# Optimization experiments

Measured on AMD Instinct MI355X. Metric: run time of the kernel, lower is better.

Reference implementation:

```python
import jax, jax.numpy as jnp
import numpy as np

D = 128          # node feature dim (input_dim)
ATT_NUM = 2      # number of attention heads (att_num)
ATT_TIMES = 2    # attention refinement iterations (att_times)
K = 1            # interact_dim from att_style 'ntn_1'
DIN2 = D * ATT_NUM   # NTN input dim = 256
FMAP = 16        # feature_map_dim
B = 8            # number of graph pairs
N = 100000       # nodes per graph
EPS = 1e-12      # F.normalize eps


def _glorot(key, shape):
    fan_in, fan_out = shape[-1], shape[-2] if len(shape) > 1 else shape[-1]
    std = np.sqrt(2.0 / (fan_in + fan_out)).astype(np.float32)
    return jax.random.normal(key, shape, dtype=jnp.float32) * std


def setup_inputs() -> dict:
    key = jax.random.key(0)
    ks = jax.random.split(key, 16)
    inp = {
        "x1": jax.random.normal(ks[0], (B, N, D), dtype=jnp.float32),
        "x2": jax.random.normal(ks[1], (B, N, D), dtype=jnp.float32),
        # Attention params (stacked over att_num heads)
        "W_att": _glorot(ks[2], (ATT_NUM, D, D)),
        "V_att": _glorot(ks[3], (ATT_NUM, K, 2 * D)),
        "Wt_att": _glorot(ks[4], (ATT_NUM, K, D, D)),
        "U_att": _glorot(ks[5], (ATT_NUM, K, 1)),
        "b_att": jax.random.normal(ks[6], (ATT_NUM, K), dtype=jnp.float32) * 0.1,
        # NTN params
        "V_ntn": _glorot(ks[7], (FMAP, 2 * DIN2)),
        "W_ntn": _glorot(ks[8], (FMAP, DIN2, DIN2)),
        "b_ntn": jax.random.normal(ks[9], (FMAP,), dtype=jnp.float32),
        # projection MLP: 16 -> 8 -> 4 -> 2 -> 1 (Linear, no bias; weight shape (out, in))
        "proj0": _glorot(ks[10], (8, 16)),
        "proj1": _glorot(ks[11], (4, 8)),
        "proj2": _glorot(ks[12], (2, 4)),
        "proj3": _glorot(ks[13], (1, 2)),
    }
    return inp


def _l1_normalize(s, axis):
    return s / jnp.maximum(jnp.sum(jnp.abs(s), axis=axis, keepdims=True), EPS)


def _attention(x, W_att, V_att, Wt_att, U_att, b_att):
    # x: (N, D)  ->  pooled graph embedding (D * ATT_NUM,)
    outs = []
    for i in range(ATT_NUM):
        xc = x
        out = None
        Va, Vb = V_att[i, :, :D], V_att[i, :, D:]   # (K, D) each
        for _ in range(ATT_TIMES):
            h = jnp.tanh(jnp.mean(xc, axis=0) @ W_att[i])        # (D,)
            # NTN-style attention scores, vectorized over all nodes
            s = xc @ Va.T + (Vb @ h)[None, :]                    # (N, K)
            s = s + jnp.einsum('nd,kde,e->nk', xc, Wt_att[i], h)
            s = s + b_att[i][None, :]
            s = _l1_normalize(s, axis=1)
            att = jax.nn.sigmoid(s) @ U_att[i]                   # (N, 1)
            out = att[:, 0] @ xc                                 # (D,)
            xc = xc * att
        outs.append(out)
    return jnp.concatenate(outs)   # (DIN2,)


def _ntn(g1, g2, V_ntn, W_ntn, b_ntn):
    # g1, g2: (DIN2,) -> (FMAP,)
    Va, Vb = V_ntn[:, :DIN2], V_ntn[:, DIN2:]
    s = Va @ g1 + Vb @ g2 + jnp.einsum('fde,d,e->f', W_ntn, g1, g2) + b_ntn
    s = s / jnp.maximum(jnp.sum(jnp.abs(s)), EPS)   # L1 normalize over the single row
    return jax.nn.relu(s)


def reference(x1, x2, W_att, V_att, Wt_att, U_att, b_att,
              V_ntn, W_ntn, b_ntn, proj0, proj1, proj2, proj3):
    def pair_fn(xa, xb):
        g1 = _attention(xa, W_att, V_att, Wt_att, U_att, b_att)
        g2 = _attention(xb, W_att, V_att, Wt_att, U_att, b_att)
        y = _ntn(g1, g2, V_ntn, W_ntn, b_ntn)      # (FMAP,)
        for Wp in (proj0, proj1, proj2, proj3):
            y = Wp @ y
        return y                                    # (1,)
    return jax.vmap(pair_fn)(x1, x2)                # (B, 1) pairwise similarity scores
```

## Files before the change

### kernel.cpp

```cpp
#include <hip/hip_runtime.h>
#include <hip/hip_bf16.h>
#include <math.h>

#define NROWS 100000
#define DIM 128
#define NGRAPH 16
#define NCHUNK 128
#define CHROWS 782
#define EPSV 1e-12f

#define SZ_SUMP (NGRAPH*NCHUNK*DIM)
#define SZ_WV   (NGRAPH*2*DIM)
#define SZ_OP   (NGRAPH*NCHUNK*2*DIM)
#define OFF_SUMP 0
#define OFF_WV1 (OFF_SUMP + SZ_SUMP)
#define OFF_C1  (OFF_WV1 + SZ_WV)
#define OFF_O1P (OFF_C1 + 32)
#define OFF_WV2 (OFF_O1P + SZ_OP)
#define OFF_C2  (OFF_WV2 + SZ_WV)
#define OFF_O2P (OFF_C2 + 32)
#define OFF_S   (OFF_O2P + SZ_OP)

typedef float v4f __attribute__((ext_vector_type(4)));

__device__ __forceinline__ const float* graph_ptr(const float* x1, const float* x2, int g) {
    return (g < 8) ? (x1 + (size_t)g * NROWS * DIM) : (x2 + (size_t)(g - 8) * NROWS * DIM);
}

__device__ __forceinline__ float4 ldnt4(const float* p) {
    v4f v = __builtin_nontemporal_load(reinterpret_cast<const v4f*>(p));
    return make_float4(v.x, v.y, v.z, v.w);
}

__device__ __forceinline__ float4 ld4(const float* p) {
    return *reinterpret_cast<const float4*>(p);
}

__device__ __forceinline__ float red16(float x) {
    int t;
    t = __builtin_amdgcn_update_dpp(0, __float_as_int(x), 0xB1, 0xF, 0xF, true);
    x += __int_as_float(t);
    t = __builtin_amdgcn_update_dpp(0, __float_as_int(x), 0x4E, 0xF, 0xF, true);
    x += __int_as_float(t);
    t = __builtin_amdgcn_update_dpp(0, __float_as_int(x), 0x141, 0xF, 0xF, true);
    x += __int_as_float(t);
    t = __builtin_amdgcn_update_dpp(0, __float_as_int(x), 0x140, 0xF, 0xF, true);
    x += __int_as_float(t);
    return x;
}

__device__ __forceinline__ float dot8(float4 v0, float4 v1, float4 w0, float4 w1) {
    float d = v0.x * w0.x;
    d = fmaf(v0.y, w0.y, d); d = fmaf(v0.z, w0.z, d); d = fmaf(v0.w, w0.w, d);
    d = fmaf(v1.x, w1.x, d); d = fmaf(v1.y, w1.y, d); d = fmaf(v1.z, w1.z, d);
    d = fmaf(v1.w, w1.w, d);
    return d;
}

__device__ __forceinline__ void acc4(float4& a, float f, float4 v) {
    a.x = fmaf(f, v.x, a.x); a.y = fmaf(f, v.y, a.y);
    a.z = fmaf(f, v.z, a.z); a.w = fmaf(f, v.w, a.w);
}

__global__ __launch_bounds__(256, 8) void k_sum(const float* __restrict__ x1,
                                                const float* __restrict__ x2,
                                                float* __restrict__ sump) {
    int g = blockIdx.x >> 7, c = blockIdx.x & (NCHUNK - 1);
    const float* xg = graph_ptr(x1, x2, g);
    int lane = threadIdx.x & 31, grp = threadIdx.x >> 5;
    int col = lane * 4;
    float ax = 0.f, ay = 0.f, az = 0.f, aw = 0.f;
    int r0 = c * CHROWS, r1 = min(r0 + CHROWS, NROWS);
    int r = r0 + grp;
    for (; r + 24 < r1; r += 32) {
        float4 a = ldnt4(xg + (size_t)r * DIM + col);
        float4 b = ldnt4(xg + (size_t)(r + 8) * DIM + col);
        float4 d = ldnt4(xg + (size_t)(r + 16) * DIM + col);
        float4 e = ldnt4(xg + (size_t)(r + 24) * DIM + col);
        ax += a.x; ay += a.y; az += a.z; aw += a.w;
        ax += b.x; ay += b.y; az += b.z; aw += b.w;
        ax += d.x; ay += d.y; az += d.z; aw += d.w;
        ax += e.x; ay += e.y; az += e.z; aw += e.w;
    }
    for (; r < r1; r += 8) {
        float4 a = ldnt4(xg + (size_t)r * DIM + col);
        ax += a.x; ay += a.y; az += a.z; aw += a.w;
    }
    __shared__ float4 lds[256];
    lds[threadIdx.x] = make_float4(ax, ay, az, aw);
    __syncthreads();
    if (threadIdx.x < 32) {
        float4 t = lds[threadIdx.x];
        for (int k = 1; k < 8; ++k) {
            float4 o = lds[k * 32 + threadIdx.x];
            t.x += o.x; t.y += o.y; t.z += o.z; t.w += o.w;
        }
        *reinterpret_cast<float4*>(sump + ((size_t)g * NCHUNK + c) * DIM + threadIdx.x * 4) = t;
    }
}

__global__ __launch_bounds__(256) void k_prep(const float* __restrict__ src, int phase,
                                              const float* __restrict__ W_att,
                                              const float* __restrict__ V_att,
                                              const float* __restrict__ Wt_att,
                                              const float* __restrict__ b_att,
                                              float* __restrict__ wv, float* __restrict__ cc) {
    int g = blockIdx.x >> 1, i = blockIdx.x & 1;
    int tid = threadIdx.x, t = tid & 127, half = tid >> 7;
    __shared__ float mean[DIM], h[DIM], red2[256];
    __shared__ float wt[DIM][DIM + 1];
    const float* Wt = Wt_att + (size_t)i * DIM * DIM;
    for (int idx = tid; idx < DIM * DIM; idx += 256)
        wt[idx >> 7][idx & 127] = Wt[idx];
    float s = 0.f;
    if (phase == 1) {
        for (int c = half; c < NCHUNK; c += 2) s += src[((size_t)g * NCHUNK + c) * DIM + t];
    } else {
        for (int c = half; c < NCHUNK; c += 2) s += src[(((size_t)g * NCHUNK + c) * 2 + i) * DIM + t];
    }
    red2[tid] = s; __syncthreads();
    if (half == 0) mean[t] = (red2[t] + red2[t + 128]) * (1.f / (float)NROWS);
    __syncthreads();
    const float* W = W_att + (size_t)i * DIM * DIM;
    float hv = 0.f;
    for (int d = half * 64; d < half * 64 + 64; ++d) hv = fmaf(mean[d], W[d * DIM + t], hv);
    red2[tid] = hv; __syncthreads();
    if (half == 0) h[t] = tanhf(red2[t] + red2[t + 128]);
    __syncthreads();
    float w = 0.f;
    for (int e = half * 64; e < half * 64 + 64; ++e) w = fmaf(wt[t][e], h[e], w);
    red2[tid] = w; __syncthreads();
    const float* Va = V_att + (size_t)i * 2 * DIM;
    if (half == 0) wv[((size_t)g * 2 + i) * DIM + t] = Va[t] + red2[t] + red2[t + 128];
    __syncthreads();
    if (half == 0) red2[t] = Va[DIM + t] * h[t];
    __syncthreads();
    for (int k = 64; k; k >>= 1) {
        if (tid < k) red2[tid] += red2[tid + k];
        __syncthreads();
    }
    if (tid == 0) cc[g * 2 + i] = red2[0] + b_att[i];
}

__device__ __forceinline__ void body2(float4 v0, float4 v1,
                                      float4 w0a, float4 w0b, float4 w1a, float4 w1b,
                                      float cc0, float cc1,
                                      float ap0, float an0, float ap1, float an1,
                                      float4& a0l, float4& a0h, float4& a1l, float4& a1h) {
    float d0 = red16(dot8(v0, v1, w0a, w0b));
    float d1 = red16(dot8(v0, v1, w1a, w1b));
    float at0 = (d0 + cc0 >= 0.f) ? ap0 : an0;
    float at1 = (d1 + cc1 >= 0.f) ? ap1 : an1;
    acc4(a0l, at0, v0); acc4(a0h, at0, v1);
    acc4(a1l, at1, v0); acc4(a1h, at1, v1);
}

__global__ __launch_bounds__(256, 6) void k_pass2(const float* __restrict__ x1,
                                                  const float* __restrict__ x2,
                                                  const float* __restrict__ wv1,
                                                  const float* __restrict__ c1,
                                                  const float* __restrict__ U_att,
                                                  float* __restrict__ o1p) {
    int g = blockIdx.x >> 7, c = blockIdx.x & (NCHUNK - 1);
    const float* xg = graph_ptr(x1, x2, g);
    int tid = threadIdx.x;
    int l16 = tid & 15, slot = tid >> 4;
    int cb = l16 * 4;
    float4 w0a = ld4(wv1 + ((size_t)g * 2 + 0) * DIM + cb);
    float4 w0b = ld4(wv1 + ((size_t)g * 2 + 0) * DIM + 64 + cb);
    float4 w1a = ld4(wv1 + ((size_t)g * 2 + 1) * DIM + cb);
    float4 w1b = ld4(wv1 + ((size_t)g * 2 + 1) * DIM + 64 + cb);
    float cc0 = c1[g * 2 + 0], cc1 = c1[g * 2 + 1];
    float u0 = U_att[0], u1 = U_att[1];
    float sp = 1.f / (1.f + expf(-1.f)), sn = 1.f / (1.f + expf(1.f));
    float ap0 = u0 * sp, an0 = u0 * sn, ap1 = u1 * sp, an1 = u1 * sn;
    float4 a0l = make_float4(0, 0, 0, 0), a0h = make_float4(0, 0, 0, 0);
    float4 a1l = make_float4(0, 0, 0, 0), a1h = make_float4(0, 0, 0, 0);
    int r0 = c * CHROWS, r1 = min(r0 + CHROWS, NROWS);
    int r = r0 + slot;
    for (; r + 16 < r1; r += 32) {
        const float* p = xg + (size_t)r * DIM + cb;
        const float* q = xg + (size_t)(r + 16) * DIM + cb;
        float4 v0 = ldnt4(p), v1 = ldnt4(p + 64);
        float4 y0 = ldnt4(q), y1 = ldnt4(q + 64);
        body2(v0, v1, w0a, w0b, w1a, w1b, cc0, cc1, ap0, an0, ap1, an1, a0l, a0h, a1l, a1h);
        body2(y0, y1, w0a, w0b, w1a, w1b, cc0, cc1, ap0, an0, ap1, an1, a0l, a0h, a1l, a1h);
    }
    for (; r < r1; r += 16) {
        const float* p = xg + (size_t)r * DIM + cb;
        float4 v0 = ldnt4(p), v1 = ldnt4(p + 64);
        body2(v0, v1, w0a, w0b, w1a, w1b, cc0, cc1, ap0, an0, ap1, an1, a0l, a0h, a1l, a1h);
    }
    __shared__ float red[2][16][DIM];
    *reinterpret_cast<float4*>(&red[0][slot][cb]) = a0l;
    *reinterpret_cast<float4*>(&red[0][slot][64 + cb]) = a0h;
    *reinterpret_cast<float4*>(&red[1][slot][cb]) = a1l;
    *reinterpret_cast<float4*>(&red[1][slot][64 + cb]) = a1h;
    __syncthreads();
    int i = tid >> 7, d = tid & 127;
    float s = 0.f;
    #pragma unroll
    for (int k = 0; k < 16; ++k) s += red[i][k][d];
    o1p[(((size_t)g * NCHUNK + c) * 2 + i) * DIM + d] = s;
}

__device__ __forceinline__ void body3(float4 v0, float4 v1,
                                      float4 wA0a, float4 wA0b, float4 wA1a, float4 wA1b,
                                      float4 wB0a, float4 wB0b, float4 wB1a, float4 wB1b,
                                      float cA0, float cA1, float cB0, float cB1,
                                      float ap0, float an0, float ap1, float an1,
                                      float4& a0l, float4& a0h, float4& a1l, float4& a1h) {
    float dA0 = red16(dot8(v0, v1, wA0a, wA0b));
    float dA1 = red16(dot8(v0, v1, wA1a, wA1b));
    float dB0 = red16(dot8(v0, v1, wB0a, wB0b));
    float dB1 = red16(dot8(v0, v1, wB1a, wB1b));
    float at10 = (dA0 + cA0 >= 0.f) ? ap0 : an0;
    float at11 = (dA1 + cA1 >= 0.f) ? ap1 : an1;
    float at20 = (fmaf(at10, dB0, cB0) >= 0.f) ? ap0 : an0;
    float at21 = (fmaf(at11, dB1, cB1) >= 0.f) ? ap1 : an1;
    float f0 = at10 * at20, f1 = at11 * at21;
    acc4(a0l, f0, v0); acc4(a0h, f0, v1);
    acc4(a1l, f1, v0); acc4(a1h, f1, v1);
}

__global__ __launch_bounds__(256, 6) void k_pass3(const float* __restrict__ x1,
                                                  const float* __restrict__ x2,
                                                  const float* __restrict__ wv1,
                                                  const float* __restrict__ c1,
                                                  const float* __restrict__ wv2,
                                                  const float* __restrict__ c2,
                                                  const float* __restrict__ U_att,
                                                  float* __restrict__ o2p) {
    int g = blockIdx.x >> 7, c = blockIdx.x & (NCHUNK - 1);
    const float* xg = graph_ptr(x1, x2, g);
    int tid = threadIdx.x;
    int l16 = tid & 15, slot = tid >> 4;
    int cb = l16 * 4;
    float4 wA0a = ld4(wv1 + ((size_t)g * 2 + 0) * DIM + cb);
    float4 wA0b = ld4(wv1 + ((size_t)g * 2 + 0) * DIM + 64 + cb);
    float4 wA1a = ld4(wv1 + ((size_t)g * 2 + 1) * DIM + cb);
    float4 wA1b = ld4(wv1 + ((size_t)g * 2 + 1) * DIM + 64 + cb);
    float4 wB0a = ld4(wv2 + ((size_t)g * 2 + 0) * DIM + cb);
    float4 wB0b = ld4(wv2 + ((size_t)g * 2 + 0) * DIM + 64 + cb);
    float4 wB1a = ld4(wv2 + ((size_t)g * 2 + 1) * DIM + cb);
    float4 wB1b = ld4(wv2 + ((size_t)g * 2 + 1) * DIM + 64 + cb);
    float cA0 = c1[g * 2 + 0], cA1 = c1[g * 2 + 1];
    float cB0 = c2[g * 2 + 0], cB1 = c2[g * 2 + 1];
    float u0 = U_att[0], u1 = U_att[1];
    float sp = 1.f / (1.f + expf(-1.f)), sn = 1.f / (1.f + expf(1.f));
    float ap0 = u0 * sp, an0 = u0 * sn, ap1 = u1 * sp, an1 = u1 * sn;
    float4 a0l = make_float4(0, 0, 0, 0), a0h = make_float4(0, 0, 0, 0);
    float4 a1l = make_float4(0, 0, 0, 0), a1h = make_float4(0, 0, 0, 0);
    int r0 = c * CHROWS, r1 = min(r0 + CHROWS, NROWS);
    int r = r0 + slot;
    for (; r + 16 < r1; r += 32) {
        const float* p = xg + (size_t)r * DIM + cb;
        const float* q = xg + (size_t)(r + 16) * DIM + cb;
        float4 v0 = ldnt4(p), v1 = ldnt4(p + 64);
        float4 y0 = ldnt4(q), y1 = ldnt4(q + 64);
        body3(v0, v1, wA0a, wA0b, wA1a, wA1b, wB0a, wB0b, wB1a, wB1b,
              cA0, cA1, cB0, cB1, ap0, an0, ap1, an1, a0l, a0h, a1l, a1h);
        body3(y0, y1, wA0a, wA0b, wA1a, wA1b, wB0a, wB0b, wB1a, wB1b,
              cA0, cA1, cB0, cB1, ap0, an0, ap1, an1, a0l, a0h, a1l, a1h);
    }
    for (; r < r1; r += 16) {
        const float* p = xg + (size_t)r * DIM + cb;
        float4 v0 = ldnt4(p), v1 = ldnt4(p + 64);
        body3(v0, v1, wA0a, wA0b, wA1a, wA1b, wB0a, wB0b, wB1a, wB1b,
              cA0, cA1, cB0, cB1, ap0, an0, ap1, an1, a0l, a0h, a1l, a1h);
    }
    __shared__ float red[2][16][DIM];
    *reinterpret_cast<float4*>(&red[0][slot][cb]) = a0l;
    *reinterpret_cast<float4*>(&red[0][slot][64 + cb]) = a0h;
    *reinterpret_cast<float4*>(&red[1][slot][cb]) = a1l;
    *reinterpret_cast<float4*>(&red[1][slot][64 + cb]) = a1h;
    __syncthreads();
    int i = tid >> 7, d = tid & 127;
    float s = 0.f;
    #pragma unroll
    for (int k = 0; k < 16; ++k) s += red[i][k][d];
    o2p[(((size_t)g * NCHUNK + c) * 2 + i) * DIM + d] = s;
}

__global__ __launch_bounds__(256) void k_ntn(const float* __restrict__ o2p,
                                             const float* __restrict__ V_ntn,
                                             const float* __restrict__ W_ntn,
                                             const float* __restrict__ b_ntn,
                                             float* __restrict__ sout) {
    int b = blockIdx.x >> 4, f = blockIdx.x & 15;
    int e = threadIdx.x;
    __shared__ float g1s[256], g2s[256], red[256];
    int i = e >> 7, d = e & 127;
    float s1 = 0.f, s2 = 0.f;
    for (int c = 0; c < NCHUNK; ++c) {
        s1 += o2p[(((size_t)b * NCHUNK + c) * 2 + i) * DIM + d];
        s2 += o2p[(((size_t)(8 + b) * NCHUNK + c) * 2 + i) * DIM + d];
    }
    g1s[e] = s1; g2s[e] = s2;
    __syncthreads();
    const float* Wf = W_ntn + (size_t)f * 256 * 256;
    float acc = 0.f;
    for (int dd = 0; dd < 256; ++dd) acc = fmaf(Wf[(size_t)dd * 256 + e], g1s[dd], acc);
    float p = acc * g2s[e];
    p = fmaf(V_ntn[(size_t)f * 512 + e], g1s[e], p);
    p = fmaf(V_ntn[(size_t)f * 512 + 256 + e], g2s[e], p);
    red[e] = p;
    __syncthreads();
    for (int k = 128; k; k >>= 1) {
        if (e < k) red[e] += red[e + k];
        __syncthreads();
    }
    if (e == 0) sout[b * 16 + f] = red[0] + b_ntn[f];
}

__global__ __launch_bounds__(64) void k_out(const float* __restrict__ sout,
                                            const float* __restrict__ p0,
                                            const float* __restrict__ p1,
                                            const float* __restrict__ p2,
                                            const float* __restrict__ p3,
                                            float* __restrict__ out) {
    int b = blockIdx.x;
    if (threadIdx.x != 0) return;
    float s[16]; float l1 = 0.f;
    for (int f = 0; f < 16; ++f) { s[f] = sout[b * 16 + f]; l1 += fabsf(s[f]); }
    float inv = 1.f / fmaxf(l1, EPSV);
    float y[16];
    for (int f = 0; f < 16; ++f) { float t = s[f] * inv; y[f] = t > 0.f ? t : 0.f; }
    float v2[4], v1[8], P[16];
    for (int j = 0; j < 4; ++j) v2[j] = p3[0] * p2[j] + p3[1] * p2[4 + j];
    for (int j = 0; j < 8; ++j) { float a = 0.f; for (int k = 0; k < 4; ++k) a = fmaf(v2[k], p1[k * 8 + j], a); v1[j] = a; }
    for (int j = 0; j < 16; ++j) { float a = 0.f; for (int k = 0; k < 8; ++k) a = fmaf(v1[k], p0[k * 16 + j], a); P[j] = a; }
    float o = 0.f;
    for (int f = 0; f < 16; ++f) o = fmaf(P[f], y[f], o);
    out[b] = o;
}

extern "C" void kernel_launch(void* const* d_in, const int* in_sizes, int n_in,
                              void* d_out, int out_size, void* d_ws, size_t ws_size,
                              hipStream_t stream) {
    const float* x1    = (const float*)d_in[0];
    const float* x2    = (const float*)d_in[1];
    const float* W_att = (const float*)d_in[2];
    const float* V_att = (const float*)d_in[3];
    const float* Wt_att= (const float*)d_in[4];
    const float* U_att = (const float*)d_in[5];
    const float* b_att = (const float*)d_in[6];
    const float* V_ntn = (const float*)d_in[7];
    const float* W_ntn = (const float*)d_in[8];
    const float* b_ntn = (const float*)d_in[9];
    const float* p0    = (const float*)d_in[10];
    const float* p1    = (const float*)d_in[11];
    const float* p2    = (const float*)d_in[12];
    const float* p3    = (const float*)d_in[13];
    float* ws  = (float*)d_ws;
    float* out = (float*)d_out;

    k_sum<<<NGRAPH * NCHUNK, 256, 0, stream>>>(x1, x2, ws + OFF_SUMP);
    k_prep<<<NGRAPH * 2, 256, 0, stream>>>(ws + OFF_SUMP, 1, W_att, V_att, Wt_att, b_att,
                                           ws + OFF_WV1, ws + OFF_C1);
    k_pass2<<<NGRAPH * NCHUNK, 256, 0, stream>>>(x1, x2, ws + OFF_WV1, ws + OFF_C1, U_att,
                                                 ws + OFF_O1P);
    k_prep<<<NGRAPH * 2, 256, 0, stream>>>(ws + OFF_O1P, 2, W_att, V_att, Wt_att, b_att,
                                           ws + OFF_WV2, ws + OFF_C2);
    k_pass3<<<NGRAPH * NCHUNK, 256, 0, stream>>>(x1, x2, ws + OFF_WV1, ws + OFF_C1,
                                                 ws + OFF_WV2, ws + OFF_C2, U_att,
                                                 ws + OFF_O2P);
    k_ntn<<<8 * 16, 256, 0, stream>>>(ws + OFF_O2P, V_ntn, W_ntn, b_ntn, ws + OFF_S);
    k_out<<<8, 64, 0, stream>>>(ws + OFF_S, p0, p1, p2, p3, out);
}
```

Before: 486.4 us.

## Process graphs in batches of four so repeated passes hit the Infinity Cache

Splits the 16 graphs into four batches and runs the sum, prep, and two attention passes per batch, so each batch (about 200 MB) can stay resident in the last-level cache across its three reads. Nontemporal loads become regular loads so the data is retained in cache. Chunk count per graph doubles and occupancy hints are removed to keep the smaller grids filled. This adds many more kernel launches, and per-launch parallelism is lower.

```diff
diff --git a/kernel.cpp b/kernel.cpp
--- a/kernel.cpp
+++ b/kernel.cpp
@@ -5,13 +5,14 @@
 #define NROWS 100000
 #define DIM 128
 #define NGRAPH 16
-#define NCHUNK 128
-#define CHROWS 782
+#define BATCH 4
+#define CH2 256
+#define CHR2 391
 #define EPSV 1e-12f
 
-#define SZ_SUMP (NGRAPH*NCHUNK*DIM)
+#define SZ_SUMP (NGRAPH*CH2*DIM)
 #define SZ_WV   (NGRAPH*2*DIM)
-#define SZ_OP   (NGRAPH*NCHUNK*2*DIM)
+#define SZ_OP   (NGRAPH*CH2*2*DIM)
 #define OFF_SUMP 0
 #define OFF_WV1 (OFF_SUMP + SZ_SUMP)
 #define OFF_C1  (OFF_WV1 + SZ_WV)
@@ -21,15 +22,8 @@
 #define OFF_O2P (OFF_C2 + 32)
 #define OFF_S   (OFF_O2P + SZ_OP)
 
-typedef float v4f __attribute__((ext_vector_type(4)));
-
 __device__ __forceinline__ const float* graph_ptr(const float* x1, const float* x2, int g) {
     return (g < 8) ? (x1 + (size_t)g * NROWS * DIM) : (x2 + (size_t)(g - 8) * NROWS * DIM);
-}
-
-__device__ __forceinline__ float4 ldnt4(const float* p) {
-    v4f v = __builtin_nontemporal_load(reinterpret_cast<const v4f*>(p));
-    return make_float4(v.x, v.y, v.z, v.w);
 }
 
 __device__ __forceinline__ float4 ld4(const float* p) {
@@ -62,28 +56,25 @@
     a.z = fmaf(f, v.z, a.z); a.w = fmaf(f, v.w, a.w);
 }
 
-__global__ __launch_bounds__(256, 8) void k_sum(const float* __restrict__ x1,
-                                                const float* __restrict__ x2,
-                                                float* __restrict__ sump) {
-    int g = blockIdx.x >> 7, c = blockIdx.x & (NCHUNK - 1);
+__global__ __launch_bounds__(256) void k_sum(const float* __restrict__ x1,
+                                             const float* __restrict__ x2,
+                                             int gbase,
+                                             float* __restrict__ sump) {
+    int g = gbase + (blockIdx.x >> 8), c = blockIdx.x & (CH2 - 1);
     const float* xg = graph_ptr(x1, x2, g);
     int lane = threadIdx.x & 31, grp = threadIdx.x >> 5;
     int col = lane * 4;
     float ax = 0.f, ay = 0.f, az = 0.f, aw = 0.f;
-    int r0 = c * CHROWS, r1 = min(r0 + CHROWS, NROWS);
+    int r0 = c * CHR2, r1 = min(r0 + CHR2, NROWS);
     int r = r0 + grp;
-    for (; r + 24 < r1; r += 32) {
-        float4 a = ldnt4(xg + (size_t)r * DIM + col);
-        float4 b = ldnt4(xg + (size_t)(r + 8) * DIM + col);
-        float4 d = ldnt4(xg + (size_t)(r + 16) * DIM + col);
-        float4 e = ldnt4(xg + (size_t)(r + 24) * DIM + col);
+    for (; r + 8 < r1; r += 16) {
+        float4 a = ld4(xg + (size_t)r * DIM + col);
+        float4 b = ld4(xg + (size_t)(r + 8) * DIM + col);
         ax += a.x; ay += a.y; az += a.z; aw += a.w;
         ax += b.x; ay += b.y; az += b.z; aw += b.w;
-        ax += d.x; ay += d.y; az += d.z; aw += d.w;
-        ax += e.x; ay += e.y; az += e.z; aw += e.w;
-    }
-    for (; r < r1; r += 8) {
-        float4 a = ldnt4(xg + (size_t)r * DIM + col);
+    }
+    if (r < r1) {
+        float4 a = ld4(xg + (size_t)r * DIM + col);
         ax += a.x; ay += a.y; az += a.z; aw += a.w;
     }
     __shared__ float4 lds[256];
@@ -95,17 +86,18 @@
             float4 o = lds[k * 32 + threadIdx.x];
             t.x += o.x; t.y += o.y; t.z += o.z; t.w += o.w;
         }
-        *reinterpret_cast<float4*>(sump + ((size_t)g * NCHUNK + c) * DIM + threadIdx.x * 4) = t;
+        *reinterpret_cast<float4*>(sump + ((size_t)g * CH2 + c) * DIM + threadIdx.x * 4) = t;
     }
 }
 
 __global__ __launch_bounds__(256) void k_prep(const float* __restrict__ src, int phase,
+                                              int gbase,
                                               const float* __restrict__ W_att,
                                               const float* __restrict__ V_att,
                                               const float* __restrict__ Wt_att,
                                               const float* __restrict__ b_att,
                                               float* __restrict__ wv, float* __restrict__ cc) {
-    int g = blockIdx.x >> 1, i = blockIdx.x & 1;
+    int g = gbase + (blockIdx.x >> 1), i = blockIdx.x & 1;
     int tid = threadIdx.x, t = tid & 127, half = tid >> 7;
     __shared__ float mean[DIM], h[DIM], red2[256];
     __shared__ float wt[DIM][DIM + 1];
@@ -114,9 +106,9 @@
         wt[idx >> 7][idx & 127] = Wt[idx];
     float s = 0.f;
     if (phase == 1) {
-        for (int c = half; c < NCHUNK; c += 2) s += src[((size_t)g * NCHUNK + c) * DIM + t];
+        for (int c = half; c < CH2; c += 2) s += src[((size_t)g * CH2 + c) * DIM + t];
     } else {
-        for (int c = half; c < NCHUNK; c += 2) s += src[(((size_t)g * NCHUNK + c) * 2 + i) * DIM + t];
+        for (int c = half; c < CH2; c += 2) s += src[(((size_t)g * CH2 + c) * 2 + i) * DIM + t];
     }
     red2[tid] = s; __syncthreads();
     if (half == 0) mean[t] = (red2[t] + red2[t + 128]) * (1.f / (float)NROWS);
@@ -155,13 +147,14 @@
     acc4(a1l, at1, v0); acc4(a1h, at1, v1);
 }
 
-__global__ __launch_bounds__(256, 6) void k_pass2(const float* __restrict__ x1,
-                                                  const float* __restrict__ x2,
-                                                  const float* __restrict__ wv1,
-                                                  const float* __restrict__ c1,
-                                                  const float* __restrict__ U_att,
-                                                  float* __restrict__ o1p) {
-    int g = blockIdx.x >> 7, c = blockIdx.x & (NCHUNK - 1);
+__global__ __launch_bounds__(256) void k_pass2(const float* __restrict__ x1,
+                                               const float* __restrict__ x2,
+                                               int gbase,
+                                               const float* __restrict__ wv1,
+                                               const float* __restrict__ c1,
+                                               const float* __restrict__ U_att,
+                                               float* __restrict__ o1p) {
+    int g = gbase + (blockIdx.x >> 8), c = blockIdx.x & (CH2 - 1);
     const float* xg = graph_ptr(x1, x2, g);
     int tid = threadIdx.x;
     int l16 = tid & 15, slot = tid >> 4;
@@ -176,19 +169,19 @@
     float ap0 = u0 * sp, an0 = u0 * sn, ap1 = u1 * sp, an1 = u1 * sn;
     float4 a0l = make_float4(0, 0, 0, 0), a0h = make_float4(0, 0, 0, 0);
     float4 a1l = make_float4(0, 0, 0, 0), a1h = make_float4(0, 0, 0, 0);
-    int r0 = c * CHROWS, r1 = min(r0 + CHROWS, NROWS);
+    int r0 = c * CHR2, r1 = min(r0 + CHR2, NROWS);
     int r = r0 + slot;
     for (; r + 16 < r1; r += 32) {
         const float* p = xg + (size_t)r * DIM + cb;
         const float* q = xg + (size_t)(r + 16) * DIM + cb;
-        float4 v0 = ldnt4(p), v1 = ldnt4(p + 64);
-        float4 y0 = ldnt4(q), y1 = ldnt4(q + 64);
+        float4 v0 = ld4(p), v1 = ld4(p + 64);
+        float4 y0 = ld4(q), y1 = ld4(q + 64);
         body2(v0, v1, w0a, w0b, w1a, w1b, cc0, cc1, ap0, an0, ap1, an1, a0l, a0h, a1l, a1h);
         body2(y0, y1, w0a, w0b, w1a, w1b, cc0, cc1, ap0, an0, ap1, an1, a0l, a0h, a1l, a1h);
     }
     for (; r < r1; r += 16) {
         const float* p = xg + (size_t)r * DIM + cb;
-        float4 v0 = ldnt4(p), v1 = ldnt4(p + 64);
+        float4 v0 = ld4(p), v1 = ld4(p + 64);
         body2(v0, v1, w0a, w0b, w1a, w1b, cc0, cc1, ap0, an0, ap1, an1, a0l, a0h, a1l, a1h);
     }
     __shared__ float red[2][16][DIM];
@@ -201,7 +194,7 @@
     float s = 0.f;
     #pragma unroll
     for (int k = 0; k < 16; ++k) s += red[i][k][d];
-    o1p[(((size_t)g * NCHUNK + c) * 2 + i) * DIM + d] = s;
+    o1p[(((size_t)g * CH2 + c) * 2 + i) * DIM + d] = s;
 }
 
 __device__ __forceinline__ void body3(float4 v0, float4 v1,
@@ -223,15 +216,16 @@
     acc4(a1l, f1, v0); acc4(a1h, f1, v1);
 }
 
-__global__ __launch_bounds__(256, 6) void k_pass3(const float* __restrict__ x1,
-                                                  const float* __restrict__ x2,
-                                                  const float* __restrict__ wv1,
-                                                  const float* __restrict__ c1,
-                                                  const float* __restrict__ wv2,
-                                                  const float* __restrict__ c2,
-                                                  const float* __restrict__ U_att,
-                                                  float* __restrict__ o2p) {
-    int g = blockIdx.x >> 7, c = blockIdx.x & (NCHUNK - 1);
+__global__ __launch_bounds__(256) void k_pass3(const float* __restrict__ x1,
+                                               const float* __restrict__ x2,
+                                               int gbase,
+                                               const float* __restrict__ wv1,
+                                               const float* __restrict__ c1,
+                                               const float* __restrict__ wv2,
+                                               const float* __restrict__ c2,
+                                               const float* __restrict__ U_att,
+                                               float* __restrict__ o2p) {
+    int g = gbase + (blockIdx.x >> 8), c = blockIdx.x & (CH2 - 1);
     const float* xg = graph_ptr(x1, x2, g);
     int tid = threadIdx.x;
     int l16 = tid & 15, slot = tid >> 4;
@@ -251,13 +245,13 @@
     float ap0 = u0 * sp, an0 = u0 * sn, ap1 = u1 * sp, an1 = u1 * sn;
     float4 a0l = make_float4(0, 0, 0, 0), a0h = make_float4(0, 0, 0, 0);
     float4 a1l = make_float4(0, 0, 0, 0), a1h = make_float4(0, 0, 0, 0);
-    int r0 = c * CHROWS, r1 = min(r0 + CHROWS, NROWS);
+    int r0 = c * CHR2, r1 = min(r0 + CHR2, NROWS);
     int r = r0 + slot;
     for (; r + 16 < r1; r += 32) {
         const float* p = xg + (size_t)r * DIM + cb;
         const float* q = xg + (size_t)(r + 16) * DIM + cb;
-        float4 v0 = ldnt4(p), v1 = ldnt4(p + 64);
-        float4 y0 = ldnt4(q), y1 = ldnt4(q + 64);
+        float4 v0 = ld4(p), v1 = ld4(p + 64);
+        float4 y0 = ld4(q), y1 = ld4(q + 64);
         body3(v0, v1, wA0a, wA0b, wA1a, wA1b, wB0a, wB0b, wB1a, wB1b,
               cA0, cA1, cB0, cB1, ap0, an0, ap1, an1, a0l, a0h, a1l, a1h);
         body3(y0, y1, wA0a, wA0b, wA1a, wA1b, wB0a, wB0b, wB1a, wB1b,
@@ -265,7 +259,7 @@
     }
     for (; r < r1; r += 16) {
         const float* p = xg + (size_t)r * DIM + cb;
-        float4 v0 = ldnt4(p), v1 = ldnt4(p + 64);
+        float4 v0 = ld4(p), v1 = ld4(p + 64);
         body3(v0, v1, wA0a, wA0b, wA1a, wA1b, wB0a, wB0b, wB1a, wB1b,
               cA0, cA1, cB0, cB1, ap0, an0, ap1, an1, a0l, a0h, a1l, a1h);
     }
@@ -279,7 +273,7 @@
     float s = 0.f;
     #pragma unroll
     for (int k = 0; k < 16; ++k) s += red[i][k][d];
-    o2p[(((size_t)g * NCHUNK + c) * 2 + i) * DIM + d] = s;
+    o2p[(((size_t)g * CH2 + c) * 2 + i) * DIM + d] = s;
 }
 
 __global__ __launch_bounds__(256) void k_ntn(const float* __restrict__ o2p,
@@ -292,9 +286,9 @@
     __shared__ float g1s[256], g2s[256], red[256];
     int i = e >> 7, d = e & 127;
     float s1 = 0.f, s2 = 0.f;
-    for (int c = 0; c < NCHUNK; ++c) {
-        s1 += o2p[(((size_t)b * NCHUNK + c) * 2 + i) * DIM + d];
-        s2 += o2p[(((size_t)(8 + b) * NCHUNK + c) * 2 + i) * DIM + d];
+    for (int c = 0; c < CH2; ++c) {
+        s1 += o2p[(((size_t)b * CH2 + c) * 2 + i) * DIM + d];
+        s2 += o2p[(((size_t)(8 + b) * CH2 + c) * 2 + i) * DIM + d];
     }
     g1s[e] = s1; g2s[e] = s2;
     __syncthreads();
@@ -355,16 +349,19 @@
     float* ws  = (float*)d_ws;
     float* out = (float*)d_out;
 
-    k_sum<<<NGRAPH * NCHUNK, 256, 0, stream>>>(x1, x2, ws + OFF_SUMP);
-    k_prep<<<NGRAPH * 2, 256, 0, stream>>>(ws + OFF_SUMP, 1, W_att, V_att, Wt_att, b_att,
-                                           ws + OFF_WV1, ws + OFF_C1);
-    k_pass2<<<NGRAPH * NCHUNK, 256, 0, stream>>>(x1, x2, ws + OFF_WV1, ws + OFF_C1, U_att,
-                                                 ws + OFF_O1P);
-    k_prep<<<NGRAPH * 2, 256, 0, stream>>>(ws + OFF_O1P, 2, W_att, V_att, Wt_att, b_att,
-                                           ws + OFF_WV2, ws + OFF_C2);
-    k_pass3<<<NGRAPH * NCHUNK, 256, 0, stream>>>(x1, x2, ws + OFF_WV1, ws + OFF_C1,
+    for (int b = 0; b < NGRAPH / BATCH; ++b) {
+        int gbase = b * BATCH;
+        k_sum<<<BATCH * CH2, 256, 0, stream>>>(x1, x2, gbase, ws + OFF_SUMP);
+        k_prep<<<BATCH * 2, 256, 0, stream>>>(ws + OFF_SUMP, 1, gbase, W_att, V_att, Wt_att,
+                                              b_att, ws + OFF_WV1, ws + OFF_C1);
+        k_pass2<<<BATCH * CH2, 256, 0, stream>>>(x1, x2, gbase, ws + OFF_WV1, ws + OFF_C1,
+                                                 U_att, ws + OFF_O1P);
+        k_prep<<<BATCH * 2, 256, 0, stream>>>(ws + OFF_O1P, 2, gbase, W_att, V_att, Wt_att,
+                                              b_att, ws + OFF_WV2, ws + OFF_C2);
+        k_pass3<<<BATCH * CH2, 256, 0, stream>>>(x1, x2, gbase, ws + OFF_WV1, ws + OFF_C1,
                                                  ws + OFF_WV2, ws + OFF_C2, U_att,
                                                  ws + OFF_O2P);
+    }
     k_ntn<<<8 * 16, 256, 0, stream>>>(ws + OFF_O2P, V_ntn, W_ntn, b_ntn, ws + OFF_S);
     k_out<<<8, 64, 0, stream>>>(ws + OFF_S, p0, p1, p2, p3, out);
 }
```

Result: slower. 720.6 us (+48.1%).
